# Kernel optimization log

Hardware: AMD Instinct MI355X
Metric: run time of the kernel (lower is better)

The kernel has to match this reference:

```python
import jax, jax.numpy as jnp
import numpy as np

N = 10000       # nodes
E = 160000      # edges
B = 100         # graphs
F_NODE = 32
F_EDGE = 16
H0, H1, H2, H3, H4, H5 = 32, 64, 128, 256, 128, 64
EPS = 1e-5


def setup_inputs() -> dict:
    key = jax.random.key(0)
    ks = jax.random.split(key, 32)

    def rn(k, shape):
        fan_in = shape[0] if len(shape) > 1 else shape[0]
        return jax.random.normal(k, shape, jnp.float32) / np.float32(np.sqrt(fan_in))

    inp = {}
    inp["x"] = jax.random.normal(ks[0], (N, F_NODE), jnp.float32)
    inp["edge_index"] = jax.random.randint(ks[1], (2, E), 0, N)
    inp["edge_attr"] = jax.random.normal(ks[2], (E, F_EDGE), jnp.float32)
    inp["batch"] = jnp.sort(jax.random.randint(ks[3], (N,), 0, B))
    # EdgeMLP: F_EDGE -> 128 -> 64 -> F_NODE*H0
    inp["We1"] = rn(ks[4], (F_EDGE, 128)); inp["be1"] = jnp.zeros((128,), jnp.float32)
    inp["We2"] = rn(ks[5], (128, 64));     inp["be2"] = jnp.zeros((64,), jnp.float32)
    inp["We3"] = rn(ks[6], (64, F_NODE * H0)); inp["be3"] = jnp.zeros((F_NODE * H0,), jnp.float32)
    # NNConv root linear + bias
    inp["Wroot"] = rn(ks[7], (F_NODE, H0)); inp["bc1"] = jnp.zeros((H0,), jnp.float32)
    # GATConv 1 (H0 -> H1, heads=1)
    inp["Wg1"] = rn(ks[8], (H0, H1)); inp["as1"] = rn(ks[9], (H1,)); inp["ad1"] = rn(ks[10], (H1,)); inp["bg1"] = jnp.zeros((H1,), jnp.float32)
    # GATConv 2 (H1 -> H2, heads=1)
    inp["Wg2"] = rn(ks[11], (H1, H2)); inp["as2"] = rn(ks[12], (H2,)); inp["ad2"] = rn(ks[13], (H2,)); inp["bg2"] = jnp.zeros((H2,), jnp.float32)
    # FC head
    inp["Wf1"] = rn(ks[14], (H2, H3)); inp["bf1"] = jnp.zeros((H3,), jnp.float32)
    inp["Wf2"] = rn(ks[15], (H3, H4)); inp["bf2"] = jnp.zeros((H4,), jnp.float32)
    inp["Wf3"] = rn(ks[16], (H4, H5)); inp["bf3"] = jnp.zeros((H5,), jnp.float32)
    return inp


def _bn(h):  # training-mode BatchNorm1d, affine = identity (default init)
    m = h.mean(axis=0)
    v = h.var(axis=0)
    return (h - m) * jax.lax.rsqrt(v + EPS)


def _seg_softmax(e, seg, n):
    m = jax.ops.segment_max(e, seg, num_segments=n)
    ex = jnp.exp(e - m[seg])
    s = jax.ops.segment_sum(ex, seg, num_segments=n)
    return ex / (s[seg] + 1e-16)


def _gat(x, src, dst, W, a_src, a_dst, b):
    n = x.shape[0]
    h = x @ W                                     # [N, F_out]
    loop = jnp.arange(n)                          # PyG add_self_loops=True
    s = jnp.concatenate([src, loop])
    d = jnp.concatenate([dst, loop])
    sc_s = h @ a_src                              # [N]
    sc_d = h @ a_dst
    e = jax.nn.leaky_relu(sc_s[s] + sc_d[d], negative_slope=0.2)
    alpha = _seg_softmax(e, d, n)                 # segment softmax over in-edges
    out = jax.ops.segment_sum(alpha[:, None] * h[s], d, num_segments=n)
    return out + b


def reference(x, edge_index, edge_attr, batch,
              We1, be1, We2, be2, We3, be3, Wroot, bc1,
              Wg1, as1, ad1, bg1, Wg2, as2, ad2, bg2,
              Wf1, bf1, Wf2, bf2, Wf3, bf3):
    src, dst = edge_index[0], edge_index[1]

    # --- NNConv: per-edge weight matrices from EdgeMLP ---
    t = jax.nn.relu(edge_attr @ We1 + be1)
    t = jax.nn.relu(t @ We2 + be2)
    theta = (t @ We3 + be3).reshape(E, F_NODE, H0)        # [E, F_in, F_out]
    msg = jnp.einsum('ef,efo->eo', x[src], theta)          # gather-matmul
    agg = jax.ops.segment_sum(msg, dst, num_segments=N)    # scatter-add (aggr='add')
    h = agg + x @ Wroot + bc1
    h = jax.nn.relu(_bn(h))

    # --- GATConv x2 ---
    h = jax.nn.relu(_bn(_gat(h, src, dst, Wg1, as1, ad1, bg1)))
    h = jax.nn.relu(_bn(_gat(h, src, dst, Wg2, as2, ad2, bg2)))

    # --- global mean pool ---
    sums = jax.ops.segment_sum(h, batch, num_segments=B)
    cnts = jax.ops.segment_sum(jnp.ones((N,), h.dtype), batch, num_segments=B)
    g = sums / jnp.maximum(cnts, 1.0)[:, None]             # [B, H2]

    # --- MLP head (dropout=Identity in eval/reference) ---
    g = jax.nn.relu(_bn(g @ Wf1 + bf1))
    g = jax.nn.relu(_bn(g @ Wf2 + bf2))
    return g @ Wf3 + bf3                                   # [B, H5]
```

## Files before the change

### kernel.cpp

```cpp
#include <hip/hip_runtime.h>

#define NN 10000
#define NE 160000
#define NGB 100

typedef __attribute__((ext_vector_type(8))) short s8v;
typedef __attribute__((ext_vector_type(4))) float f4v;
typedef __attribute__((ext_vector_type(2))) _Float16 h2v;
typedef __attribute__((ext_vector_type(8))) _Float16 h8v;

static __device__ __forceinline__ float lrelu(float v){ return v > 0.f ? v : 0.2f*v; }
static __device__ __forceinline__ unsigned short f2bf(float f){
  unsigned u = __float_as_uint(f);
  u += 0x7fffu + ((u >> 16) & 1u);
  return (unsigned short)(u >> 16);
}
static __device__ __forceinline__ float bf2f(unsigned short h){
  return __uint_as_float(((unsigned)h) << 16);
}
static __device__ __forceinline__ unsigned pkh(float a, float b){
  auto h = __builtin_amdgcn_cvt_pkrtz(a, b);
  return __builtin_bit_cast(unsigned, h);
}
static __device__ __forceinline__ unsigned short f2h(float f){
  _Float16 h = (_Float16)f;
  return __builtin_bit_cast(unsigned short, h);
}
static __device__ __forceinline__ float h2f(unsigned short u){
  return (float)__builtin_bit_cast(_Float16, u);
}

__global__ __launch_bounds__(256) void k_prep(const int* __restrict__ src, const int* __restrict__ dst,
    const int* __restrict__ batch,
    const float* __restrict__ We1, const float* __restrict__ be1,
    const float* __restrict__ We2, const float* __restrict__ We3,
    int* deg_src, int* deg_dst, int* starts,
    unsigned short* __restrict__ W1p, unsigned short* __restrict__ W2p,
    unsigned short* __restrict__ W3h, unsigned short* __restrict__ W3l){
  int i = blockIdx.x*256 + threadIdx.x;
  if (i < NE){ atomicAdd(&deg_src[src[i]],1); atomicAdd(&deg_dst[dst[i]],1); }
  if (i <= NN){
    int cur  = (i==NN) ? NGB : batch[i];
    int prev = (i==0)  ? -1  : batch[i-1];
    for (int b=prev+1; b<=cur; b++) if (b<=NGB) starts[b]=i;
  }
  int tid = threadIdx.x;
  if (blockIdx.x == 32){
    for (int idx=tid; idx<512; idx+=256){
      int j=idx>>6, l=idx&63, col=l&15, g=l>>4;
      int out = j*16+col;
      #pragma unroll
      for (int jj=0;jj<8;jj++){
        int k = g*8+jj;
        float v = (k<16) ? We1[k*128+out] : (k==16 ? be1[out] : 0.f);
        W1p[idx*8+jj] = f2bf(v);
      }
    }
    for (int idx=tid; idx<1024; idx+=256){
      int ft=idx>>6, l=idx&63, col=l&15, g=l>>4;
      int t=ft>>2, jo=ft&3;
      int out = jo*16+col;
      #pragma unroll
      for (int jj=0;jj<8;jj++){
        int k = t*32+g*8+jj;
        W2p[idx*8+jj] = f2bf(We2[k*64+out]);
      }
    }
  } else if (blockIdx.x < 32){
    int idx = blockIdx.x*256 + tid;
    int jt = idx>>6, l = idx&63;
    int j = jt*16 + (l&15);
    int f0 = (l>>4)*8;
    int k = j>>5, o = j&31;
    #pragma unroll
    for (int jj=0;jj<8;jj++){
      float v = We3[(size_t)k*1024 + (size_t)(f0+jj)*32 + o];
      unsigned short h = f2bf(v);
      float r = v - bf2f(h);
      W3h[(size_t)idx*8+jj] = h;
      W3l[(size_t)idx*8+jj] = f2bf(r);
    }
  }
}

__global__ __launch_bounds__(1024) void k_scan(const int* __restrict__ deg_src, const int* __restrict__ deg_dst,
                                               int* rp_src, int* rp_dst){
  const int* deg = (blockIdx.x==0) ? deg_src : deg_dst;
  int* rp = (blockIdx.x==0) ? rp_src : rp_dst;
  __shared__ int part[1024];
  int tid = threadIdx.x;
  const int per = (NN + 1023)/1024;
  int base = tid*per;
  int s = 0;
  for (int i=0;i<per;i++){ int idx=base+i; if (idx<NN) s += deg[idx]; }
  part[tid]=s; __syncthreads();
  for (int off=1; off<1024; off<<=1){
    int v = part[tid];
    int add = (tid>=off) ? part[tid-off] : 0;
    __syncthreads();
    part[tid] = v + add;
    __syncthreads();
  }
  int run = (tid==0) ? 0 : part[tid-1];
  for (int i=0;i<per;i++){ int idx=base+i; if (idx<NN){ rp[idx]=run; run += deg[idx]; } }
  if (tid==1023) rp[NN] = part[1023];
}

__global__ __launch_bounds__(256) void k_fill(const int* __restrict__ src, const int* __restrict__ dst,
                       const int* __restrict__ rp_src, const int* __restrict__ rp_dst,
                       int* fill_src, int* fill_dst, int* pos_src, int* dstp, int* srcd){
  int i = blockIdx.x*256 + threadIdx.x;
  if (i < NE){
    int s=src[i], d=dst[i];
    int p=rp_src[s]+atomicAdd(&fill_src[s],1); pos_src[i]=p; dstp[p]=d;
    int q=rp_dst[d]+atomicAdd(&fill_dst[d],1); srcd[q]=s;
  }
}

__global__ __launch_bounds__(256) void k_big(const float* __restrict__ ea,
    const unsigned short* __restrict__ W1p, const unsigned short* __restrict__ W2p,
    const float* __restrict__ be2, const int* __restrict__ pos_src, unsigned* __restrict__ t2b,
    const float* __restrict__ x,
    const unsigned short* __restrict__ W3h, const unsigned short* __restrict__ W3l,
    unsigned* __restrict__ Yp,
    const float* __restrict__ be3, const float* __restrict__ Wroot, const float* __restrict__ bc1,
    float* __restrict__ xb, float* __restrict__ agg){
  __shared__ unsigned short st1[4*2048];
  int bid = blockIdx.x;
  int tid=threadIdx.x, wave=tid>>6, lane=tid&63;
  const f4v fz = {0.f,0.f,0.f,0.f};
  if (bid < 625){
    int c = lane&15, g = lane>>4;
    s8v w1f[8], w2f[16];
    #pragma unroll
    for (int j=0;j<8;j++)  w1f[j] = *(const s8v*)(W1p + (size_t)(j*64+lane)*8);
    #pragma unroll
    for (int q=0;q<16;q++) w2f[q] = *(const s8v*)(W2p + (size_t)(q*64+lane)*8);
    float be2v[16];
    #pragma unroll
    for (int jo=0;jo<4;jo++)
      #pragma unroll
      for (int r=0;r<4;r++) be2v[jo*4+r] = be2[jo*16+g*4+r];
    char* myld = (char*)(st1 + wave*2048);
    for (int base = bid*64; base < NE; base += 625*64){
      int e0 = base + wave*16;
      s8v eaf = {0,0,0,0,0,0,0,0};
      if (g < 2){
        const float* p = ea + (size_t)(e0+c)*16 + g*8;
        float4 a = *(const float4*)p;
        float4 b = *(const float4*)(p+4);
        eaf[0]=(short)f2bf(a.x); eaf[1]=(short)f2bf(a.y); eaf[2]=(short)f2bf(a.z); eaf[3]=(short)f2bf(a.w);
        eaf[4]=(short)f2bf(b.x); eaf[5]=(short)f2bf(b.y); eaf[6]=(short)f2bf(b.z); eaf[7]=(short)f2bf(b.w);
      } else if (g == 2){
        eaf[0] = (short)0x3f80;
      }
      f4v acc1[8];
      #pragma unroll
      for (int j=0;j<8;j++)
        acc1[j] = __builtin_amdgcn_mfma_f32_16x16x32_bf16(w1f[j], eaf, fz, 0, 0, 0);
      #pragma unroll
      for (int j=0;j<8;j++){
        unsigned lo = (unsigned)f2bf(fmaxf(acc1[j][0],0.f)) | ((unsigned)f2bf(fmaxf(acc1[j][1],0.f))<<16);
        unsigned hi = (unsigned)f2bf(fmaxf(acc1[j][2],0.f)) | ((unsigned)f2bf(fmaxf(acc1[j][3],0.f))<<16);
        unsigned off = (unsigned)(c*256 + ((j*32 + g*8) ^ (c<<4)));
        *(uint2*)(myld + off) = make_uint2(lo, hi);
      }
      __syncthreads();
      f4v acc2[4];
      #pragma unroll
      for (int jo=0;jo<4;jo++) acc2[jo] = fz;
      #pragma unroll
      for (int t=0;t<4;t++){
        unsigned off = (unsigned)(c*256 + ((t*64 + g*16) ^ (c<<4)));
        s8v b2 = *(const s8v*)(myld + off);
        #pragma unroll
        for (int jo=0;jo<4;jo++)
          acc2[jo] = __builtin_amdgcn_mfma_f32_16x16x32_bf16(w2f[t*4+jo], b2, acc2[jo], 0, 0, 0);
      }
      int pos = pos_src[e0+c];
      unsigned* orow = t2b + (size_t)pos*32;
      #pragma unroll
      for (int jo=0;jo<4;jo++){
        float v0 = fmaxf(acc2[jo][0] + be2v[jo*4+0], 0.f);
        float v1 = fmaxf(acc2[jo][1] + be2v[jo*4+1], 0.f);
        float v2 = fmaxf(acc2[jo][2] + be2v[jo*4+2], 0.f);
        float v3 = fmaxf(acc2[jo][3] + be2v[jo*4+3], 0.f);
        *(uint2*)(orow + jo*8 + g*2) = make_uint2(pkh(v0,v1), pkh(v2,v3));
      }
      __syncthreads();
    }
  } else if (bid < 938){
    int c = lane&15, g = lane>>4;
    int tile = (bid-625)*2 + (wave>>1);
    if (tile >= 625) return;
    int jhalf = wave&1;
    int n = tile*16 + c;
    const float* xr = x + (size_t)n*32 + g*8;
    float4 xa = *(const float4*)xr;
    float4 xc = *(const float4*)(xr+4);
    float xv[8] = {xa.x,xa.y,xa.z,xa.w,xc.x,xc.y,xc.z,xc.w};
    s8v bh, bl;
    #pragma unroll
    for (int jj=0;jj<8;jj++){
      unsigned short h = f2bf(xv[jj]);
      bh[jj] = (short)h;
      bl[jj] = (short)f2bf(xv[jj] - bf2f(h));
    }
    unsigned* Yrow = Yp + (size_t)n*1024;
    for (int grp=0; grp<4; grp++){
      int jt_g0 = jhalf*64 + grp*16;
      int kpg = jhalf*4 + grp;
      uint4 Q[2][4];
      #pragma unroll
      for (int a=0; a<4; a++){
        #pragma unroll
        for (int b=0; b<2; b++){
          int jt_lo = jt_g0 + 4*a + b;
          int jt_hi = jt_lo + 2;
          s8v AhL = *(const s8v*)(W3h + (size_t)(jt_lo*64 + lane)*8);
          s8v AlL = *(const s8v*)(W3l + (size_t)(jt_lo*64 + lane)*8);
          f4v aL = __builtin_amdgcn_mfma_f32_16x16x32_bf16(AhL, bl, fz, 0, 0, 0);
          aL = __builtin_amdgcn_mfma_f32_16x16x32_bf16(AlL, bh, aL, 0, 0, 0);
          aL = __builtin_amdgcn_mfma_f32_16x16x32_bf16(AhL, bh, aL, 0, 0, 0);
          s8v AhH = *(const s8v*)(W3h + (size_t)(jt_hi*64 + lane)*8);
          s8v AlH = *(const s8v*)(W3l + (size_t)(jt_hi*64 + lane)*8);
          f4v aH = __builtin_amdgcn_mfma_f32_16x16x32_bf16(AhH, bl, fz, 0, 0, 0);
          aH = __builtin_amdgcn_mfma_f32_16x16x32_bf16(AlH, bh, aH, 0, 0, 0);
          aH = __builtin_amdgcn_mfma_f32_16x16x32_bf16(AhH, bh, aH, 0, 0, 0);
          #pragma unroll
          for (int r=0;r<4;r++){
            unsigned pv = pkh(aL[r], aH[r]);
            if (a==0) Q[b][r].x = pv;
            else if (a==1) Q[b][r].y = pv;
            else if (a==2) Q[b][r].z = pv;
            else Q[b][r].w = pv;
          }
        }
      }
      #pragma unroll
      for (int b=0;b<2;b++)
        #pragma unroll
        for (int r=0;r<4;r++){
          int o = b*16 + g*4 + r;
          *(uint4*)(Yrow + kpg*128 + o*4) = Q[b][r];
        }
    }
  } else {
    __shared__ __align__(16) float sx[8][32];
    int b2 = bid - 938;
    int oo = tid & 31, nn = tid >> 5;
    float wb[32], wr[32];
    #pragma unroll
    for (int f=0;f<32;f++){ wb[f]=be3[f*32+oo]; wr[f]=Wroot[f*32+oo]; }
    float bcv = bc1[oo];
    int per = (1250 + 63)/64;
    int g0 = b2*per, g1 = min(g0+per, 1250);
    for (int gi=g0; gi<g1; gi++){
      int nb = gi*8;
      __syncthreads();
      sx[tid>>5][tid&31] = x[(size_t)nb*32 + tid];
      __syncthreads();
      float a1=0.f, a2=0.f;
      #pragma unroll
      for (int f4=0;f4<8;f4++){
        float4 xvv = *(const float4*)(&sx[nn][f4*4]);
        a1 += xvv.x*wb[f4*4+0]+xvv.y*wb[f4*4+1]+xvv.z*wb[f4*4+2]+xvv.w*wb[f4*4+3];
        a2 += xvv.x*wr[f4*4+0]+xvv.y*wr[f4*4+1]+xvv.z*wr[f4*4+2]+xvv.w*wr[f4*4+3];
      }
      xb[(size_t)(nb+nn)*32+oo] = a1;
      agg[(size_t)(nb+nn)*32+oo] = a2 + bcv;
    }
  }
}

__global__ __launch_bounds__(256) void k_msg4(const unsigned* __restrict__ Yp,
    const float* __restrict__ xb, const unsigned* __restrict__ t2b,
    const int* __restrict__ rp_src, const int* __restrict__ dstp,
    float* __restrict__ agg){
  int tid=threadIdx.x, w=tid>>6, lane=tid&63;
  int c = lane&15, g = lane>>4;
  int gw = blockIdx.x*4 + w, stride = gridDim.x*4;
  const f4v fz = {0.f,0.f,0.f,0.f};
  for (int n=gw; n<NN; n+=stride){
    int beg=rp_src[n], end=rp_src[n+1];
    if (beg==end) continue;
    const unsigned* Yr = Yp + (size_t)n*1024;
    h8v B[2][2];
    #pragma unroll
    for (int kt=0;kt<2;kt++)
      #pragma unroll
      for (int jn=0;jn<2;jn++)
        B[kt][jn] = __builtin_bit_cast(h8v, *(const uint4*)(Yr + (kt*4+g)*128 + (jn*16+c)*4));
    float xq0 = xb[(size_t)n*32 + c];
    float xq1 = xb[(size_t)n*32 + c + 16];
    for (int eb=beg; eb<end; eb+=16){
      const unsigned* tr = t2b + (size_t)(eb + c)*32;
      h8v A0 = __builtin_bit_cast(h8v, *(const uint4*)(tr + g*4));
      h8v A1 = __builtin_bit_cast(h8v, *(const uint4*)(tr + 16 + g*4));
      f4v acc0 = __builtin_amdgcn_mfma_f32_16x16x32_f16(A0, B[0][0], fz, 0, 0, 0);
      acc0 = __builtin_amdgcn_mfma_f32_16x16x32_f16(A1, B[1][0], acc0, 0, 0, 0);
      f4v acc1 = __builtin_amdgcn_mfma_f32_16x16x32_f16(A0, B[0][1], fz, 0, 0, 0);
      acc1 = __builtin_amdgcn_mfma_f32_16x16x32_f16(A1, B[1][1], acc1, 0, 0, 0);
      #pragma unroll
      for (int r=0;r<4;r++){
        int p = eb + g*4 + r;
        if (p < end){
          int d = dstp[p];
          float* ap = agg + (size_t)d*32;
          unsafeAtomicAdd(ap + c,      acc0[r] + xq0);
          unsafeAtomicAdd(ap + c + 16, acc1[r] + xq1);
        }
      }
    }
  }
}

__global__ __launch_bounds__(256) void k_stats(const float* __restrict__ buf, int nrows, int ncols,
                                               float* __restrict__ stats){
  int tid = threadIdx.x;
  int c  = tid % ncols;
  int r0 = tid / ncols;
  int rp = 256 / ncols;
  float s1=0.f, s2=0.f;
  for (long long base=(long long)blockIdx.x*rp; base<nrows; base+=(long long)gridDim.x*rp){
    int r = (int)base + r0;
    if (r < nrows){
      float v = buf[(size_t)r*ncols + c];
      s1 += v; s2 += v*v;
    }
  }
  __shared__ float A[256], B[256];
  A[tid]=s1; B[tid]=s2; __syncthreads();
  if (tid < ncols){
    float t1=0.f, t2=0.f;
    for (int gg=0; gg<256/ncols; gg++){ t1 += A[gg*ncols+tid]; t2 += B[gg*ncols+tid]; }
    atomicAdd(&stats[tid], t1);
    atomicAdd(&stats[ncols+tid], t2);
  }
}

template<int FIN, int FOUT>
__global__ __launch_bounds__(256) void k_gat_linear(const float* __restrict__ raw,
    const float* __restrict__ stats, const float* __restrict__ W,
    const float* __restrict__ avs, const float* __restrict__ avd,
    unsigned short* __restrict__ hWh, float* __restrict__ sc_s, float* __restrict__ sc_d){
  __shared__ float sW[FIN*FOUT];
  __shared__ float sA[FOUT], sD[FOUT];
  __shared__ float sScale[FIN], sShift[FIN];
  __shared__ float sIn[4][FIN];
  int tid = threadIdx.x;
  for (int i=tid;i<FIN*FOUT;i+=256) sW[i]=W[i];
  if (tid<FOUT){ sA[tid]=avs[tid]; sD[tid]=avd[tid]; }
  if (tid<FIN){
    float m = stats[tid]*(1.f/NN);
    float v = stats[FIN+tid]*(1.f/NN) - m*m;
    float s = rsqrtf(v + 1e-5f);
    sScale[tid]=s; sShift[tid]=-m*s;
  }
  __syncthreads();
  int wave=tid>>6, lane=tid&63;
  for (int nb = blockIdx.x*4; nb < NN; nb += gridDim.x*4){
    int n = nb + wave;
    bool act = n < NN;
    if (act){
      for (int ff=lane; ff<FIN; ff+=64){
        float vv = raw[(size_t)n*FIN+ff]*sScale[ff]+sShift[ff];
        sIn[wave][ff] = fmaxf(vv, 0.f);
      }
    }
    __syncthreads();
    if (act){
      float out0=0.f, out1=0.f;
      #pragma unroll
      for (int ff=0; ff<FIN; ff++){
        float xv = sIn[wave][ff];
        out0 += xv*sW[ff*FOUT+lane];
        if constexpr (FOUT > 64) out1 += xv*sW[ff*FOUT+lane+64];
      }
      hWh[(size_t)n*FOUT + lane] = f2h(out0);
      float ps = out0*sA[lane], pd = out0*sD[lane];
      if constexpr (FOUT > 64){
        hWh[(size_t)n*FOUT + lane + 64] = f2h(out1);
        ps += out1*sA[lane+64]; pd += out1*sD[lane+64];
      }
      #pragma unroll
      for (int off=32;off>0;off>>=1){ ps += __shfl_down(ps,off); pd += __shfl_down(pd,off); }
      if (lane==0){ sc_s[n]=ps; sc_d[n]=pd; }
    }
    __syncthreads();
  }
}

template<int F>
__global__ __launch_bounds__(256) void k_gat_attn5(const unsigned short* __restrict__ hWh,
    const float* __restrict__ sc_s, const float* __restrict__ sc_d,
    const int* __restrict__ rp_dst, const int* __restrict__ srcd,
    const float* __restrict__ bias, float* __restrict__ outraw){
  int tid=threadIdx.x, w=tid>>6, lane=tid&63;
  int gw = blockIdx.x*4 + w, stride = gridDim.x*4;
  for (int n=gw; n<NN; n+=stride){
    int beg=rp_dst[n], end=rp_dst[n+1];
    float scd = sc_d[n];
    float M=-3e38f, S=0.f, acc0=0.f, acc1=0.f;
    for (int base=beg; base<end; base+=64){
      int nb = min(64, end-base);
      float sc=-3e38f; int si=0;
      if (lane<nb){ si = srcd[base+lane]; sc = lrelu(sc_s[si]+scd); }
      float cm=sc;
      #pragma unroll
      for (int off=32;off>0;off>>=1) cm = fmaxf(cm, __shfl_xor(cm,off));
      float Mn = fmaxf(M, cm);
      float p = (lane<nb) ? __expf(sc-Mn) : 0.f;
      float ps=p;
      #pragma unroll
      for (int off=32;off>0;off>>=1) ps += __shfl_xor(ps,off);
      float scale = __expf(M-Mn);
      S = S*scale + ps;
      acc0*=scale; acc1*=scale;
      int jj=0;
      for (; jj+4<=nb; jj+=4){
        float p0=__shfl(p,jj), p1=__shfl(p,jj+1), p2=__shfl(p,jj+2), p3=__shfl(p,jj+3);
        int   q0=__shfl(si,jj), q1=__shfl(si,jj+1), q2=__shfl(si,jj+2), q3=__shfl(si,jj+3);
        if constexpr (F==128){
          unsigned u0 = *(const unsigned*)(hWh + (size_t)q0*128 + 2*lane);
          unsigned u1 = *(const unsigned*)(hWh + (size_t)q1*128 + 2*lane);
          unsigned u2 = *(const unsigned*)(hWh + (size_t)q2*128 + 2*lane);
          unsigned u3 = *(const unsigned*)(hWh + (size_t)q3*128 + 2*lane);
          acc0 += p0*h2f((unsigned short)(u0&0xffffu)); acc1 += p0*h2f((unsigned short)(u0>>16));
          acc0 += p1*h2f((unsigned short)(u1&0xffffu)); acc1 += p1*h2f((unsigned short)(u1>>16));
          acc0 += p2*h2f((unsigned short)(u2&0xffffu)); acc1 += p2*h2f((unsigned short)(u2>>16));
          acc0 += p3*h2f((unsigned short)(u3&0xffffu)); acc1 += p3*h2f((unsigned short)(u3>>16));
        } else {
          float v0 = h2f(hWh[(size_t)q0*64+lane]);
          float v1 = h2f(hWh[(size_t)q1*64+lane]);
          float v2 = h2f(hWh[(size_t)q2*64+lane]);
          float v3 = h2f(hWh[(size_t)q3*64+lane]);
          acc0 += p0*v0 + p1*v1 + p2*v2 + p3*v3;
        }
      }
      for (; jj<nb; jj++){
        float pj=__shfl(p,jj); int qj=__shfl(si,jj);
        if constexpr (F==128){
          unsigned u = *(const unsigned*)(hWh + (size_t)qj*128 + 2*lane);
          acc0 += pj*h2f((unsigned short)(u&0xffffu));
          acc1 += pj*h2f((unsigned short)(u>>16));
        } else {
          acc0 += pj*h2f(hWh[(size_t)qj*64+lane]);
        }
      }
      M = Mn;
    }
    float sself = lrelu(sc_s[n]+scd);
    float Mn = fmaxf(M, sself);
    float scale = __expf(M-Mn);
    float pself = __expf(sself-Mn);
    S = S*scale + pself;
    acc0*=scale; acc1*=scale;
    float inv = 1.f/(S+1e-16f);
    if constexpr (F==128){
      unsigned u = *(const unsigned*)(hWh + (size_t)n*128 + 2*lane);
      acc0 += pself*h2f((unsigned short)(u&0xffffu));
      acc1 += pself*h2f((unsigned short)(u>>16));
      float ox = acc0*inv + bias[2*lane];
      float oy = acc1*inv + bias[2*lane+1];
      *(float2*)(outraw + (size_t)n*128 + 2*lane) = make_float2(ox, oy);
    } else {
      acc0 += pself*h2f(hWh[(size_t)n*64+lane]);
      outraw[(size_t)n*64+lane] = acc0*inv + bias[lane];
    }
  }
}

__global__ __launch_bounds__(256) void k_poolhead1(const float* __restrict__ h2raw,
    const float* __restrict__ stats, const int* __restrict__ starts,
    const float* __restrict__ Wf1, const float* __restrict__ bf1,
    float* __restrict__ g1, float* __restrict__ statsH1){
  __shared__ float sc[128], sh[128], red[256], sg[128];
  int b=blockIdx.x, t=threadIdx.x;
  if (t<128){
    float m = stats[t]*(1.f/NN);
    float v = stats[128+t]*(1.f/NN) - m*m;
    float s = rsqrtf(v+1e-5f);
    sc[t]=s; sh[t]=-m*s;
  }
  __syncthreads();
  int s0=starts[b], s1=starts[b+1];
  int f=t&127, half=t>>7;
  float acc=0.f;
  for (int n=s0+half;n<s1;n+=2){
    float v = h2raw[(size_t)n*128+f]*sc[f]+sh[f];
    acc += fmaxf(v,0.f);
  }
  red[t]=acc; __syncthreads();
  if (half==0){
    int cnt = s1-s0;
    sg[f] = (red[f]+red[128+f]) / fmaxf((float)cnt, 1.f);
  }
  __syncthreads();
  float a = bf1[t];
  #pragma unroll 4
  for (int k=0;k<128;k++) a += sg[k]*Wf1[k*256+t];
  g1[b*256+t]=a;
  atomicAdd(&statsH1[t], a);
  atomicAdd(&statsH1[256+t], a*a);
}

__global__ __launch_bounds__(256) void k_head2(const float* __restrict__ g1,
    const float* __restrict__ stats, const float* __restrict__ Wf2,
    const float* __restrict__ bf2, float* __restrict__ g2, float* __restrict__ statsH2){
  __shared__ float sin_[256];
  int r=blockIdx.x, t=threadIdx.x;
  float m = stats[t]*(1.f/NGB);
  float v = stats[256+t]*(1.f/NGB) - m*m;
  float val = (g1[r*256+t]-m)*rsqrtf(v+1e-5f);
  sin_[t]=fmaxf(val,0.f);
  __syncthreads();
  if (t<128){
    float acc=bf2[t];
    #pragma unroll 4
    for (int k=0;k<256;k++) acc += sin_[k]*Wf2[k*128+t];
    g2[r*128+t]=acc;
    atomicAdd(&statsH2[t], acc);
    atomicAdd(&statsH2[128+t], acc*acc);
  }
}

__global__ __launch_bounds__(256) void k_head3(const float* __restrict__ g2,
    const float* __restrict__ stats, const float* __restrict__ Wf3,
    const float* __restrict__ bf3, float* __restrict__ out){
  __shared__ float sin_[128];
  int r=blockIdx.x, t=threadIdx.x;
  if (t<128){
    float m = stats[t]*(1.f/NGB);
    float v = stats[128+t]*(1.f/NGB) - m*m;
    float val = (g2[r*128+t]-m)*rsqrtf(v+1e-5f);
    sin_[t]=fmaxf(val,0.f);
  }
  __syncthreads();
  if (t<64){
    float acc=bf3[t];
    #pragma unroll 4
    for (int k=0;k<128;k++) acc += sin_[k]*Wf3[k*64+t];
    out[r*64+t]=acc;
  }
}

extern "C" void kernel_launch(void* const* d_in, const int* in_sizes, int n_in,
                              void* d_out, int out_size, void* d_ws, size_t ws_size,
                              hipStream_t stream){
  const float* x    = (const float*)d_in[0];
  const int*   ei   = (const int*)d_in[1];
  const float* ea   = (const float*)d_in[2];
  const int*   batch= (const int*)d_in[3];
  const float* We1=(const float*)d_in[4];  const float* be1=(const float*)d_in[5];
  const float* We2=(const float*)d_in[6];  const float* be2=(const float*)d_in[7];
  const float* We3=(const float*)d_in[8];  const float* be3=(const float*)d_in[9];
  const float* Wroot=(const float*)d_in[10]; const float* bc1=(const float*)d_in[11];
  const float* Wg1=(const float*)d_in[12]; const float* as1=(const float*)d_in[13];
  const float* ad1=(const float*)d_in[14]; const float* bg1=(const float*)d_in[15];
  const float* Wg2=(const float*)d_in[16]; const float* as2=(const float*)d_in[17];
  const float* ad2=(const float*)d_in[18]; const float* bg2=(const float*)d_in[19];
  const float* Wf1=(const float*)d_in[20]; const float* bf1=(const float*)d_in[21];
  const float* Wf2=(const float*)d_in[22]; const float* bf2=(const float*)d_in[23];
  const float* Wf3=(const float*)d_in[24]; const float* bf3=(const float*)d_in[25];
  (void)in_sizes; (void)n_in; (void)out_size; (void)ws_size;
  float* out = (float*)d_out;
  char* ws = (char*)d_ws;
  const int* srcA = ei;
  const int* dstA = ei + NE;

  size_t off = 0;
  auto take = [&](size_t bytes)->size_t{ size_t r = off; off += (bytes + 255) & ~(size_t)255; return r; };
  size_t o_deg_src = take(NN*4), o_deg_dst = take(NN*4);
  size_t o_fill_src = take(NN*4), o_fill_dst = take(NN*4);
  size_t o_stats0 = take(2*32*4), o_stats1 = take(2*64*4), o_stats2 = take(2*128*4);
  size_t o_statsH1 = take(2*256*4), o_statsH2 = take(2*128*4);
  size_t zero_bytes = off;
  size_t o_rp_src = take((NN+1)*4), o_rp_dst = take((NN+1)*4);
  size_t o_pos_src = take((size_t)NE*4);
  size_t o_dstp = take((size_t)NE*4);
  size_t o_srcd = take((size_t)NE*4);
  size_t o_starts = take((NGB+1)*4);
  size_t o_W1p = take(4096*2);
  size_t o_W2p = take(8192*2);
  size_t o_W3h = take((size_t)128*64*8*2);
  size_t o_W3l = take((size_t)128*64*8*2);
  size_t o_t2b = take((size_t)(NE+16)*32*4);
  size_t o_Yp  = take((size_t)NN*1024*4);
  size_t o_xb  = take((size_t)NN*32*4);
  size_t o_agg = take((size_t)NN*32*4);
  size_t o_hW1 = take((size_t)NN*64*2);
  size_t o_scs1 = take(NN*4), o_scd1 = take(NN*4);
  size_t o_h1  = take((size_t)NN*64*4);
  size_t o_hW2 = take((size_t)NN*128*2);
  size_t o_scs2 = take(NN*4), o_scd2 = take(NN*4);
  size_t o_h2  = take((size_t)NN*128*4);
  size_t o_g1  = take(NGB*256*4);
  size_t o_g2  = take(NGB*128*4);

  #define WF(o) ((float*)(ws + (o)))
  #define WI(o) ((int*)(ws + (o)))
  #define WU(o) ((unsigned short*)(ws + (o)))
  #define WW(o) ((unsigned*)(ws + (o)))

  (void)hipMemsetAsync(ws, 0, zero_bytes, stream);
  k_prep<<<625,256,0,stream>>>(srcA,dstA,batch,We1,be1,We2,We3,
                               WI(o_deg_src),WI(o_deg_dst),WI(o_starts),
                               WU(o_W1p),WU(o_W2p),WU(o_W3h),WU(o_W3l));
  k_scan<<<2,1024,0,stream>>>(WI(o_deg_src),WI(o_deg_dst),WI(o_rp_src),WI(o_rp_dst));
  k_fill<<<625,256,0,stream>>>(srcA,dstA,WI(o_rp_src),WI(o_rp_dst),
                               WI(o_fill_src),WI(o_fill_dst),
                               WI(o_pos_src),WI(o_dstp),WI(o_srcd));
  k_big<<<1002,256,0,stream>>>(ea,WU(o_W1p),WU(o_W2p),be2,WI(o_pos_src),WW(o_t2b),
                               x,WU(o_W3h),WU(o_W3l),WW(o_Yp),
                               be3,Wroot,bc1,WF(o_xb),WF(o_agg));
  k_msg4<<<2500,256,0,stream>>>(WW(o_Yp),WF(o_xb),WW(o_t2b),WI(o_rp_src),WI(o_dstp),WF(o_agg));

  k_stats<<<64,256,0,stream>>>(WF(o_agg),NN,32,WF(o_stats0));
  k_gat_linear<32,64><<<640,256,0,stream>>>(WF(o_agg),WF(o_stats0),Wg1,as1,ad1,
                                            WU(o_hW1),WF(o_scs1),WF(o_scd1));
  k_gat_attn5<64><<<2500,256,0,stream>>>(WU(o_hW1),WF(o_scs1),WF(o_scd1),
                                         WI(o_rp_dst),WI(o_srcd),bg1,WF(o_h1));
  k_stats<<<64,256,0,stream>>>(WF(o_h1),NN,64,WF(o_stats1));
  k_gat_linear<64,128><<<640,256,0,stream>>>(WF(o_h1),WF(o_stats1),Wg2,as2,ad2,
                                             WU(o_hW2),WF(o_scs2),WF(o_scd2));
  k_gat_attn5<128><<<2500,256,0,stream>>>(WU(o_hW2),WF(o_scs2),WF(o_scd2),
                                          WI(o_rp_dst),WI(o_srcd),bg2,WF(o_h2));
  k_stats<<<64,256,0,stream>>>(WF(o_h2),NN,128,WF(o_stats2));

  k_poolhead1<<<NGB,256,0,stream>>>(WF(o_h2),WF(o_stats2),WI(o_starts),Wf1,bf1,
                                    WF(o_g1),WF(o_statsH1));
  k_head2<<<NGB,256,0,stream>>>(WF(o_g1),WF(o_statsH1),Wf2,bf2,WF(o_g2),WF(o_statsH2));
  k_head3<<<NGB,256,0,stream>>>(WF(o_g2),WF(o_statsH2),Wf3,bf3,out);
}
```

Measured before the change: 263.3 us.

## Fuse final stats and MLP head into one persistent kernel with grid barriers

Replaces the last stats kernel and the three head kernels with a single 100-block kernel. Inside it, software grid barriers built on atomic counters separate the BN-statistics reduction, pooling plus first linear layer, second layer and third layer. The goal is to remove four kernel launch gaps on the serial tail. The cost is spin-wait barriers that rely on all 100 blocks being resident at once, and a stats pass that now runs on only 100 blocks instead of 64×256 threads.

```diff
diff --git a/kernel.cpp b/kernel.cpp
--- a/kernel.cpp
+++ b/kernel.cpp
@@ -28,6 +28,20 @@
 }
 static __device__ __forceinline__ float h2f(unsigned short u){
   return (float)__builtin_bit_cast(_Float16, u);
+}
+static __device__ __forceinline__ void stf(float* p, float v){
+  __hip_atomic_store(p, v, __ATOMIC_RELAXED, __HIP_MEMORY_SCOPE_SYSTEM);
+}
+static __device__ __forceinline__ void gridbar(int* bar, int target){
+  __syncthreads();
+  if (threadIdx.x == 0){
+    asm volatile("s_waitcnt vmcnt(0)" ::: "memory");
+    __hip_atomic_fetch_add(bar, 1, __ATOMIC_RELAXED, __HIP_MEMORY_SCOPE_SYSTEM);
+    while (__hip_atomic_load(bar, __ATOMIC_RELAXED, __HIP_MEMORY_SCOPE_SYSTEM) < target)
+      __builtin_amdgcn_s_sleep(8);
+    asm volatile("" ::: "memory");
+  }
+  __syncthreads();
 }
 
 __global__ __launch_bounds__(256) void k_prep(const int* __restrict__ src, const int* __restrict__ dst,
@@ -471,77 +485,95 @@
   }
 }
 
-__global__ __launch_bounds__(256) void k_poolhead1(const float* __restrict__ h2raw,
-    const float* __restrict__ stats, const int* __restrict__ starts,
+__global__ __launch_bounds__(256) void k_tail(const float* __restrict__ h2raw,
+    const int* __restrict__ starts,
     const float* __restrict__ Wf1, const float* __restrict__ bf1,
-    float* __restrict__ g1, float* __restrict__ statsH1){
-  __shared__ float sc[128], sh[128], red[256], sg[128];
+    const float* __restrict__ Wf2, const float* __restrict__ bf2,
+    const float* __restrict__ Wf3, const float* __restrict__ bf3,
+    float* __restrict__ stats2, float* __restrict__ statsH1, float* __restrict__ statsH2,
+    float* __restrict__ g1, float* __restrict__ g2, float* __restrict__ out,
+    int* __restrict__ bar){
+  __shared__ float sm0[256], sm1[256];
   int b=blockIdx.x, t=threadIdx.x;
-  if (t<128){
-    float m = stats[t]*(1.f/NN);
-    float v = stats[128+t]*(1.f/NN) - m*m;
-    float s = rsqrtf(v+1e-5f);
-    sc[t]=s; sh[t]=-m*s;
-  }
-  __syncthreads();
-  int s0=starts[b], s1=starts[b+1];
-  int f=t&127, half=t>>7;
-  float acc=0.f;
-  for (int n=s0+half;n<s1;n+=2){
-    float v = h2raw[(size_t)n*128+f]*sc[f]+sh[f];
-    acc += fmaxf(v,0.f);
-  }
-  red[t]=acc; __syncthreads();
-  if (half==0){
-    int cnt = s1-s0;
-    sg[f] = (red[f]+red[128+f]) / fmaxf((float)cnt, 1.f);
-  }
-  __syncthreads();
-  float a = bf1[t];
-  #pragma unroll 4
-  for (int k=0;k<128;k++) a += sg[k]*Wf1[k*256+t];
-  g1[b*256+t]=a;
-  atomicAdd(&statsH1[t], a);
-  atomicAdd(&statsH1[256+t], a*a);
-}
-
-__global__ __launch_bounds__(256) void k_head2(const float* __restrict__ g1,
-    const float* __restrict__ stats, const float* __restrict__ Wf2,
-    const float* __restrict__ bf2, float* __restrict__ g2, float* __restrict__ statsH2){
-  __shared__ float sin_[256];
-  int r=blockIdx.x, t=threadIdx.x;
-  float m = stats[t]*(1.f/NGB);
-  float v = stats[256+t]*(1.f/NGB) - m*m;
-  float val = (g1[r*256+t]-m)*rsqrtf(v+1e-5f);
-  sin_[t]=fmaxf(val,0.f);
-  __syncthreads();
-  if (t<128){
-    float acc=bf2[t];
+  {
+    int c = t & 127, r0 = t >> 7;
+    float s1=0.f, s2=0.f;
+    for (int base=b*2; base<NN; base+=100*2){
+      int r = base + r0;
+      if (r < NN){
+        float v = h2raw[(size_t)r*128 + c];
+        s1 += v; s2 += v*v;
+      }
+    }
+    sm0[t]=s1; sm1[t]=s2; __syncthreads();
+    if (t < 128){
+      atomicAdd(&stats2[t],     sm0[t]+sm0[128+t]);
+      atomicAdd(&stats2[128+t], sm1[t]+sm1[128+t]);
+    }
+  }
+  gridbar(bar, 100);
+  {
+    __shared__ float sc[128], sh[128], red[256], sg[128];
+    if (t<128){
+      float m = stats2[t]*(1.f/NN);
+      float v = stats2[128+t]*(1.f/NN) - m*m;
+      float s = rsqrtf(v+1e-5f);
+      sc[t]=s; sh[t]=-m*s;
+    }
+    __syncthreads();
+    int s0=starts[b], s1=starts[b+1];
+    int f=t&127, half=t>>7;
+    float acc=0.f;
+    for (int n=s0+half;n<s1;n+=2){
+      float v = h2raw[(size_t)n*128+f]*sc[f]+sh[f];
+      acc += fmaxf(v,0.f);
+    }
+    red[t]=acc; __syncthreads();
+    if (half==0){
+      int cnt = s1-s0;
+      sg[f] = (red[f]+red[128+f]) / fmaxf((float)cnt, 1.f);
+    }
+    __syncthreads();
+    float a = bf1[t];
     #pragma unroll 4
-    for (int k=0;k<256;k++) acc += sin_[k]*Wf2[k*128+t];
-    g2[r*128+t]=acc;
-    atomicAdd(&statsH2[t], acc);
-    atomicAdd(&statsH2[128+t], acc*acc);
-  }
-}
-
-__global__ __launch_bounds__(256) void k_head3(const float* __restrict__ g2,
-    const float* __restrict__ stats, const float* __restrict__ Wf3,
-    const float* __restrict__ bf3, float* __restrict__ out){
-  __shared__ float sin_[128];
-  int r=blockIdx.x, t=threadIdx.x;
-  if (t<128){
-    float m = stats[t]*(1.f/NGB);
-    float v = stats[128+t]*(1.f/NGB) - m*m;
-    float val = (g2[r*128+t]-m)*rsqrtf(v+1e-5f);
+    for (int k=0;k<128;k++) a += sg[k]*Wf1[k*256+t];
+    stf(&g1[b*256+t], a);
+    atomicAdd(&statsH1[t], a);
+    atomicAdd(&statsH1[256+t], a*a);
+  }
+  gridbar(bar, 200);
+  {
+    __shared__ float sin_[256];
+    float m = statsH1[t]*(1.f/NGB);
+    float v = statsH1[256+t]*(1.f/NGB) - m*m;
+    float val = (g1[b*256+t]-m)*rsqrtf(v+1e-5f);
     sin_[t]=fmaxf(val,0.f);
-  }
-  __syncthreads();
-  if (t<64){
-    float acc=bf3[t];
-    #pragma unroll 4
-    for (int k=0;k<128;k++) acc += sin_[k]*Wf3[k*64+t];
-    out[r*64+t]=acc;
+    __syncthreads();
+    if (t<128){
+      float acc=bf2[t];
+      #pragma unroll 4
+      for (int k=0;k<256;k++) acc += sin_[k]*Wf2[k*128+t];
+      stf(&g2[b*128+t], acc);
+      atomicAdd(&statsH2[t], acc);
+      atomicAdd(&statsH2[128+t], acc*acc);
+    }
+  }
+  gridbar(bar, 300);
+  {
+    __shared__ float sin_[128];
+    if (t<128){
+      float m = statsH2[t]*(1.f/NGB);
+      float v = statsH2[128+t]*(1.f/NGB) - m*m;
+      float val = (g2[b*128+t]-m)*rsqrtf(v+1e-5f);
+      sin_[t]=fmaxf(val,0.f);
+    }
+    __syncthreads();
+    if (t<64){
+      float acc=bf3[t];
+      #pragma unroll 4
+      for (int k=0;k<128;k++) acc += sin_[k]*Wf3[k*64+t];
+      out[b*64+t]=acc;
+    }
   }
 }
 
@@ -575,6 +607,7 @@
   size_t o_fill_src = take(NN*4), o_fill_dst = take(NN*4);
   size_t o_stats0 = take(2*32*4), o_stats1 = take(2*64*4), o_stats2 = take(2*128*4);
   size_t o_statsH1 = take(2*256*4), o_statsH2 = take(2*128*4);
+  size_t o_bar = take(256);
   size_t zero_bytes = off;
   size_t o_rp_src = take((NN+1)*4), o_rp_dst = take((NN+1)*4);
   size_t o_pos_src = take((size_t)NE*4);
@@ -626,10 +659,8 @@
                                              WU(o_hW2),WF(o_scs2),WF(o_scd2));
   k_gat_attn5<128><<<2500,256,0,stream>>>(WU(o_hW2),WF(o_scs2),WF(o_scd2),
                                           WI(o_rp_dst),WI(o_srcd),bg2,WF(o_h2));
-  k_stats<<<64,256,0,stream>>>(WF(o_h2),NN,128,WF(o_stats2));
-
-  k_poolhead1<<<NGB,256,0,stream>>>(WF(o_h2),WF(o_stats2),WI(o_starts),Wf1,bf1,
-                                    WF(o_g1),WF(o_statsH1));
-  k_head2<<<NGB,256,0,stream>>>(WF(o_g1),WF(o_statsH1),Wf2,bf2,WF(o_g2),WF(o_statsH2));
-  k_head3<<<NGB,256,0,stream>>>(WF(o_g2),WF(o_statsH2),Wf3,bf3,out);
-}
+
+  k_tail<<<NGB,256,0,stream>>>(WF(o_h2),WI(o_starts),Wf1,bf1,Wf2,bf2,Wf3,bf3,
+                               WF(o_stats2),WF(o_statsH1),WF(o_statsH2),
+                               WF(o_g1),WF(o_g2),out,WI(o_bar));
+}
```

After: 257.1 us. 2.4% less time.
